# Performance work log

Measured on AMD Instinct MI355X. Metric: run time of the kernel, lower is better.

Reference implementation:

```python
import jax, jax.numpy as jnp
import numpy as np

# Faithful JAX translation of fastmax_function with mask=True, p=1, normalize=0.
# In that branch the torch code sets temperature = 1 and uses a0 = a1 = 1.

def setup_inputs() -> dict:
    key = jax.random.key(0)
    kq, kk, kv = jax.random.split(key, 3)
    b, h, n, d = 2, 8, 8192, 32
    q = jax.random.normal(kq, (b, h, n, d), dtype=jnp.float32)
    k = jax.random.normal(kk, (b, h, n, d), dtype=jnp.float32)
    v = jax.random.normal(kv, (b, h, n, d), dtype=jnp.float32)
    return {"q": q, "k": k, "v": v}


def reference(q, k, v):
    # q, k, v: (b, h, n, d); causal (mask=True), p=1, a0=a1=1, temperature=1
    b, h, n, d = q.shape
    # first term: running sum of values
    first = jnp.cumsum(v, axis=2)                                  # (b,h,n,d)
    # second term: q_i . (sum_{j<=i} k_j v_j^T)
    kv = jnp.einsum('bhnd,bhne->bhnde', k, v)                      # (b,h,n,d,d)
    kv_cs = jnp.cumsum(kv, axis=2)                                 # (b,h,n,d,d)
    second = jnp.einsum('bhnd,bhnde->bhne', q, kv_cs)              # (b,h,n,d)
    # denominator: i + q_i . (sum_{j<=i} k_j)
    k_cs = jnp.cumsum(k, axis=2)                                   # (b,h,n,d)
    div1 = jnp.arange(1, n + 1, dtype=q.dtype)                     # (n,)
    div2 = jnp.einsum('bhnd,bhnd->bhn', q, k_cs)                   # (b,h,n)
    div = (div1[None, None, :] + div2)[..., None]                  # (b,h,n,1)
    return (first + second) / div
```

## Files before the change

### kernel.cpp

```cpp
#include <hip/hip_runtime.h>


#define D      32
#define C      64
#define NCHUNK 128
#define BH     16
#define NSEQ   8192
#define STATE  1088

typedef __attribute__((ext_vector_type(8))) short bf16x8;
typedef __attribute__((ext_vector_type(4))) float f32x4;

__device__ __forceinline__ unsigned short f2bf(float x) {
  union { float f; unsigned u; } c; c.f = x;
  unsigned r = (c.u + 0x7FFFu + ((c.u >> 16) & 1u)) >> 16;
  return (unsigned short)r;
}

__global__ __launch_bounds__(256) void chunk_state_kernel(
    const float* __restrict__ k, const float* __restrict__ v,
    float* __restrict__ states) {
  int blk = blockIdx.x;
  int bh  = blk >> 7;
  int c   = blk & 127;
  size_t off = ((size_t)bh * NSEQ + (size_t)c * C) * D;
  const float* kp = k + off;
  const float* vp = v + off;

  __shared__ __align__(16) unsigned short kT[D * 72];
  __shared__ __align__(16) unsigned short vT[D * 72];
  __shared__ __align__(16) float psK[256];
  __shared__ __align__(16) float psV[256];

  int t = threadIdx.x;
  int e = t & 31;
  float sk = 0.f, sv = 0.f;
  for (int r = 0; r < 8; ++r) {
    int idx = t + r * 256;
    int j = idx >> 5;
    float kvv = kp[idx], vvv = vp[idx];
    kT[e * 72 + j] = f2bf(kvv);
    vT[e * 72 + j] = f2bf(vvv);
    sk += kvv; sv += vvv;
  }
  psK[t] = sk; psV[t] = sv;
  __syncthreads();

  int lane = t & 63, w = t >> 6;
  int m16 = lane & 15, quad = lane >> 4;
  int mb = w >> 1, nb = w & 1;
  f32x4 acc = {0.f, 0.f, 0.f, 0.f};
#pragma unroll
  for (int kb = 0; kb < 2; ++kb) {
    bf16x8 a = *(const bf16x8*)&kT[(16 * mb + m16) * 72 + kb * 32 + quad * 8];
    bf16x8 b = *(const bf16x8*)&vT[(16 * nb + m16) * 72 + kb * 32 + quad * 8];
    acc = __builtin_amdgcn_mfma_f32_16x16x32_bf16(a, b, acc, 0, 0, 0);
  }
  float* st = states + (size_t)blk * STATE;
#pragma unroll
  for (int reg = 0; reg < 4; ++reg) {
    int d1 = 16 * mb + quad * 4 + reg;
    int d2 = 16 * nb + m16;
    st[d1 * 32 + d2] = acc[reg];
  }
  if (t < 64) {
    int ee = t & 31;
    float s = 0.f;
    if (t < 32) {
#pragma unroll
      for (int g = 0; g < 8; ++g) s += psK[ee + 32 * g];
      st[1024 + ee] = s;
    } else {
#pragma unroll
      for (int g = 0; g < 8; ++g) s += psV[ee + 32 * g];
      st[1056 + ee] = s;
    }
  }
}

__global__ __launch_bounds__(256) void scan_kernel(float* __restrict__ states) {
  int gidx = blockIdx.x * 256 + threadIdx.x;
  int bh = gidx / STATE;
  int e  = gidx % STATE;
  float* base = states + (size_t)bh * NCHUNK * STATE + e;
  float a = 0.f;
#pragma unroll 1
  for (int c0 = 0; c0 < NCHUNK; c0 += 16) {
    float s[16];
#pragma unroll
    for (int r = 0; r < 16; ++r) s[r] = base[(size_t)(c0 + r) * STATE];
#pragma unroll
    for (int r = 0; r < 16; ++r) { float tv = s[r]; s[r] = a; a += tv; }
#pragma unroll
    for (int r = 0; r < 16; ++r) base[(size_t)(c0 + r) * STATE] = s[r];
  }
}

__global__ __launch_bounds__(256) void output_kernel(
    const float* __restrict__ q, const float* __restrict__ k,
    const float* __restrict__ v, const float* __restrict__ states,
    float* __restrict__ out) {
  int blk = blockIdx.x;
  int bh  = blk >> 7;
  int c   = blk & 127;
  size_t off = ((size_t)bh * NSEQ + (size_t)c * C) * D;
  const float* qp = q + off;
  const float* kp = k + off;
  const float* vp = v + off;
  const float* st = states + (size_t)blk * STATE;

  __shared__ __align__(16) unsigned short qbf[C * 40];
  __shared__ __align__(16) unsigned short kbf[C * 40];
  __shared__ __align__(16) unsigned short vTbf[D * 72];
  __shared__ __align__(16) unsigned short kvTbf[D * 40];
  __shared__ __align__(16) unsigned short Tbf[C * 72];
  __shared__ __align__(16) float q_s[C * 36];
  __shared__ __align__(16) float kc_s[C * 36];
  __shared__ __align__(16) float gtot[8 * 32];
  __shared__ __align__(16) float kpre_s[D], vpre_s[D], invdiv_s[C];

  int t = threadIdx.x;
  int e = t & 31;

  for (int z = t; z < (C * 72) / 8; z += 256)
    ((uint4*)Tbf)[z] = make_uint4(0, 0, 0, 0);
  for (int r = 0; r < 8; ++r) {
    int idx = t + r * 256;
    int j = idx >> 5;
    float qv = qp[idx], kv = kp[idx], vv = vp[idx];
    q_s[j * 36 + e]  = qv;  qbf[j * 40 + e] = f2bf(qv);
    kc_s[j * 36 + e] = kv;  kbf[j * 40 + e] = f2bf(kv);
    vTbf[e * 72 + j] = f2bf(vv);
  }
  for (int r = 0; r < 4; ++r) {
    int idx = t + r * 256;
    int dd = idx >> 5;
    kvTbf[e * 40 + dd] = f2bf(st[idx]);
  }
  if (t < 32)      kpre_s[t]      = st[1024 + t];
  else if (t < 64) vpre_s[t - 32] = st[1024 + t];
  __syncthreads();

  int lane = t & 63, w = t >> 6;
  int m16 = lane & 15, quad = lane >> 4;

  const bf16x8 aQ = *(const bf16x8*)&qbf[(16 * w + m16) * 40 + quad * 8];
  for (int jb = 0; jb <= w; ++jb) {
    bf16x8 bK = *(const bf16x8*)&kbf[(16 * jb + m16) * 40 + quad * 8];
    f32x4 cS = {0.f, 0.f, 0.f, 0.f};
    cS = __builtin_amdgcn_mfma_f32_16x16x32_bf16(aQ, bK, cS, 0, 0, 0);
    int jcol = 16 * jb + m16;
#pragma unroll
    for (int reg = 0; reg < 4; ++reg) {
      int i = 16 * w + quad * 4 + reg;
      float tv = (jcol <= i) ? (1.f + cS[reg]) : 0.f;
      Tbf[i * 72 + jcol] = f2bf(tv);
    }
  }
  int rg = t >> 5;
  float vals[8];
  {
    float run = 0.f;
#pragma unroll
    for (int r = 0; r < 8; ++r) {
      vals[r] = kc_s[(rg * 8 + r) * 36 + e];
      run += vals[r];
    }
    gtot[rg * 32 + e] = run;
  }
  __syncthreads();

  {
    float offv = kpre_s[e];
    for (int g = 0; g < rg; ++g) offv += gtot[g * 32 + e];
    float cacc = offv;
#pragma unroll
    for (int r = 0; r < 8; ++r) {
      cacc += vals[r];
      kc_s[(rg * 8 + r) * 36 + e] = cacc;
    }
  }
  __syncthreads();

  if (t < 64) {
    int i = t;
    float dp = 0.f;
#pragma unroll
    for (int d4 = 0; d4 < 8; ++d4) {
      float4 qv = *(const float4*)&q_s[i * 36 + 4 * d4];
      float4 kc = *(const float4*)&kc_s[i * 36 + 4 * d4];
      dp += qv.x * kc.x + qv.y * kc.y + qv.z * kc.z + qv.w * kc.w;
    }
    invdiv_s[i] = 1.f / ((float)(c * C + i + 1) + dp);
  }
  f32x4 o0 = {0.f, 0.f, 0.f, 0.f}, o1 = {0.f, 0.f, 0.f, 0.f};
  {
    bf16x8 b0 = *(const bf16x8*)&kvTbf[(m16)      * 40 + quad * 8];
    bf16x8 b1 = *(const bf16x8*)&kvTbf[(16 + m16) * 40 + quad * 8];
    o0 = __builtin_amdgcn_mfma_f32_16x16x32_bf16(aQ, b0, o0, 0, 0, 0);
    o1 = __builtin_amdgcn_mfma_f32_16x16x32_bf16(aQ, b1, o1, 0, 0, 0);
  }
  int kbcnt = (w >= 2) ? 2 : 1;
  for (int kb = 0; kb < kbcnt; ++kb) {
    bf16x8 aT = *(const bf16x8*)&Tbf[(16 * w + m16) * 72 + kb * 32 + quad * 8];
    bf16x8 b0 = *(const bf16x8*)&vTbf[(m16)      * 72 + kb * 32 + quad * 8];
    bf16x8 b1 = *(const bf16x8*)&vTbf[(16 + m16) * 72 + kb * 32 + quad * 8];
    o0 = __builtin_amdgcn_mfma_f32_16x16x32_bf16(aT, b0, o0, 0, 0, 0);
    o1 = __builtin_amdgcn_mfma_f32_16x16x32_bf16(aT, b1, o1, 0, 0, 0);
  }
  __syncthreads();

#pragma unroll
  for (int reg = 0; reg < 4; ++reg) {
    int i = 16 * w + quad * 4 + reg;
    float id = invdiv_s[i];
    int e0 = m16, e1 = 16 + m16;
    out[off + (size_t)i * D + e0] = (vpre_s[e0] + o0[reg]) * id;
    out[off + (size_t)i * D + e1] = (vpre_s[e1] + o1[reg]) * id;
  }
}

extern "C" void kernel_launch(void* const* d_in, const int* in_sizes, int n_in,
                              void* d_out, int out_size, void* d_ws, size_t ws_size,
                              hipStream_t stream) {
  const float* q = (const float*)d_in[0];
  const float* k = (const float*)d_in[1];
  const float* v = (const float*)d_in[2];
  float* out    = (float*)d_out;
  float* states = (float*)d_ws;

  chunk_state_kernel<<<BH * NCHUNK, 256, 0, stream>>>(k, v, states);
  scan_kernel<<<(BH * STATE) / 256, 256, 0, stream>>>(states);
  output_kernel<<<BH * NCHUNK, 256, 0, stream>>>(q, k, v, states, out);
}
```

Before: 113.3 us.

## Vectorize global loads with float4 and permute value columns for paired float2 stores

Both chunk kernels now load q/k/v and states as float4 vectors with a row/column-group thread mapping instead of scalar strided loads, and write bf16 tiles to shared memory in vector form. The value and kv-state columns are permuted so each lane's two MFMA output columns are adjacent, which allows float2 output stores. The scan kernel is unrolled to 32 chunks per batch, and the partial-sum reduction is reorganized to match the new mapping. The aim is fewer, wider memory transactions, at the cost of a slightly more complex indexing scheme.

```diff
diff --git a/kernel.cpp b/kernel.cpp
--- a/kernel.cpp
+++ b/kernel.cpp
@@ -10,6 +10,7 @@
 
 typedef __attribute__((ext_vector_type(8))) short bf16x8;
 typedef __attribute__((ext_vector_type(4))) float f32x4;
+typedef __attribute__((ext_vector_type(4))) unsigned short u16x4;
 
 __device__ __forceinline__ unsigned short f2bf(float x) {
   union { float f; unsigned u; } c; c.f = x;
@@ -17,33 +18,39 @@
   return (unsigned short)r;
 }
 
+__device__ __forceinline__ int permcol(int e) {
+  return (e & 1) ? (16 + (e >> 1)) : (e >> 1);
+}
+
 __global__ __launch_bounds__(256) void chunk_state_kernel(
     const float* __restrict__ k, const float* __restrict__ v,
     float* __restrict__ states) {
   int blk = blockIdx.x;
-  int bh  = blk >> 7;
-  int c   = blk & 127;
-  size_t off = ((size_t)bh * NSEQ + (size_t)c * C) * D;
-  const float* kp = k + off;
-  const float* vp = v + off;
+  const float4* kp = (const float4*)k + (size_t)blk * 512;
+  const float4* vp = (const float4*)v + (size_t)blk * 512;
 
   __shared__ __align__(16) unsigned short kT[D * 72];
   __shared__ __align__(16) unsigned short vT[D * 72];
-  __shared__ __align__(16) float psK[256];
-  __shared__ __align__(16) float psV[256];
-
-  int t = threadIdx.x;
-  int e = t & 31;
-  float sk = 0.f, sv = 0.f;
-  for (int r = 0; r < 8; ++r) {
-    int idx = t + r * 256;
-    int j = idx >> 5;
-    float kvv = kp[idx], vvv = vp[idx];
-    kT[e * 72 + j] = f2bf(kvv);
-    vT[e * 72 + j] = f2bf(vvv);
-    sk += kvv; sv += vvv;
-  }
-  psK[t] = sk; psV[t] = sv;
+  __shared__ __align__(16) float4 psK[256];
+  __shared__ __align__(16) float4 psV[256];
+
+  int t  = threadIdx.x;
+  int j0 = t >> 3;
+  int cb = (t & 7) * 4;
+  float4 kA = kp[t], kB = kp[t + 256];
+  float4 vA = vp[t], vB = vp[t + 256];
+
+  const float* ka = &kA.x; const float* kb = &kB.x;
+  const float* va = &vA.x; const float* vb = &vB.x;
+#pragma unroll
+  for (int cc = 0; cc < 4; ++cc) {
+    kT[(cb + cc) * 72 + j0]      = f2bf(ka[cc]);
+    kT[(cb + cc) * 72 + j0 + 32] = f2bf(kb[cc]);
+    vT[(cb + cc) * 72 + j0]      = f2bf(va[cc]);
+    vT[(cb + cc) * 72 + j0 + 32] = f2bf(vb[cc]);
+  }
+  psK[t] = make_float4(kA.x + kB.x, kA.y + kB.y, kA.z + kB.z, kA.w + kB.w);
+  psV[t] = make_float4(vA.x + vB.x, vA.y + vB.y, vA.z + vB.z, vA.w + vB.w);
   __syncthreads();
 
   int lane = t & 63, w = t >> 6;
@@ -51,9 +58,9 @@
   int mb = w >> 1, nb = w & 1;
   f32x4 acc = {0.f, 0.f, 0.f, 0.f};
 #pragma unroll
-  for (int kb = 0; kb < 2; ++kb) {
-    bf16x8 a = *(const bf16x8*)&kT[(16 * mb + m16) * 72 + kb * 32 + quad * 8];
-    bf16x8 b = *(const bf16x8*)&vT[(16 * nb + m16) * 72 + kb * 32 + quad * 8];
+  for (int kb2 = 0; kb2 < 2; ++kb2) {
+    bf16x8 a = *(const bf16x8*)&kT[(16 * mb + m16) * 72 + kb2 * 32 + quad * 8];
+    bf16x8 b = *(const bf16x8*)&vT[(16 * nb + m16) * 72 + kb2 * 32 + quad * 8];
     acc = __builtin_amdgcn_mfma_f32_16x16x32_bf16(a, b, acc, 0, 0, 0);
   }
   float* st = states + (size_t)blk * STATE;
@@ -65,16 +72,11 @@
   }
   if (t < 64) {
     int ee = t & 31;
+    const float* ps = (t < 32) ? (const float*)psK : (const float*)psV;
     float s = 0.f;
-    if (t < 32) {
-#pragma unroll
-      for (int g = 0; g < 8; ++g) s += psK[ee + 32 * g];
-      st[1024 + ee] = s;
-    } else {
-#pragma unroll
-      for (int g = 0; g < 8; ++g) s += psV[ee + 32 * g];
-      st[1056 + ee] = s;
-    }
+#pragma unroll
+    for (int m = 0; m < 32; ++m) s += ps[ee + 32 * m];
+    st[1024 + ((t < 32) ? ee : 32 + ee)] = s;
   }
 }
 
@@ -85,14 +87,14 @@
   float* base = states + (size_t)bh * NCHUNK * STATE + e;
   float a = 0.f;
 #pragma unroll 1
-  for (int c0 = 0; c0 < NCHUNK; c0 += 16) {
-    float s[16];
-#pragma unroll
-    for (int r = 0; r < 16; ++r) s[r] = base[(size_t)(c0 + r) * STATE];
-#pragma unroll
-    for (int r = 0; r < 16; ++r) { float tv = s[r]; s[r] = a; a += tv; }
-#pragma unroll
-    for (int r = 0; r < 16; ++r) base[(size_t)(c0 + r) * STATE] = s[r];
+  for (int c0 = 0; c0 < NCHUNK; c0 += 32) {
+    float s[32];
+#pragma unroll
+    for (int r = 0; r < 32; ++r) s[r] = base[(size_t)(c0 + r) * STATE];
+#pragma unroll
+    for (int r = 0; r < 32; ++r) { float tv = s[r]; s[r] = a; a += tv; }
+#pragma unroll
+    for (int r = 0; r < 32; ++r) base[(size_t)(c0 + r) * STATE] = s[r];
   }
 }
 
@@ -101,13 +103,12 @@
     const float* __restrict__ v, const float* __restrict__ states,
     float* __restrict__ out) {
   int blk = blockIdx.x;
-  int bh  = blk >> 7;
   int c   = blk & 127;
-  size_t off = ((size_t)bh * NSEQ + (size_t)c * C) * D;
-  const float* qp = q + off;
-  const float* kp = k + off;
-  const float* vp = v + off;
-  const float* st = states + (size_t)blk * STATE;
+  size_t off = (size_t)blk * (C * D);
+  const float4* qp4 = (const float4*)q + (size_t)blk * 512;
+  const float4* kp4 = (const float4*)k + (size_t)blk * 512;
+  const float4* vp4 = (const float4*)v + (size_t)blk * 512;
+  const float4* st4 = (const float4*)(states + (size_t)blk * STATE);
 
   __shared__ __align__(16) unsigned short qbf[C * 40];
   __shared__ __align__(16) unsigned short kbf[C * 40];
@@ -119,26 +120,45 @@
   __shared__ __align__(16) float gtot[8 * 32];
   __shared__ __align__(16) float kpre_s[D], vpre_s[D], invdiv_s[C];
 
-  int t = threadIdx.x;
-  int e = t & 31;
+  int t  = threadIdx.x;
+  int j0 = t >> 3;
+  int cb = (t & 7) * 4;
+
+  float4 qA = qp4[t], qB = qp4[t + 256];
+  float4 kA = kp4[t], kB = kp4[t + 256];
+  float4 vA = vp4[t], vB = vp4[t + 256];
+  float4 sv = st4[t];
+  float4 tail = make_float4(0.f, 0.f, 0.f, 0.f);
+  if (t < 16) tail = st4[256 + t];
 
   for (int z = t; z < (C * 72) / 8; z += 256)
     ((uint4*)Tbf)[z] = make_uint4(0, 0, 0, 0);
-  for (int r = 0; r < 8; ++r) {
-    int idx = t + r * 256;
-    int j = idx >> 5;
-    float qv = qp[idx], kv = kp[idx], vv = vp[idx];
-    q_s[j * 36 + e]  = qv;  qbf[j * 40 + e] = f2bf(qv);
-    kc_s[j * 36 + e] = kv;  kbf[j * 40 + e] = f2bf(kv);
-    vTbf[e * 72 + j] = f2bf(vv);
-  }
-  for (int r = 0; r < 4; ++r) {
-    int idx = t + r * 256;
-    int dd = idx >> 5;
-    kvTbf[e * 40 + dd] = f2bf(st[idx]);
-  }
-  if (t < 32)      kpre_s[t]      = st[1024 + t];
-  else if (t < 64) vpre_s[t - 32] = st[1024 + t];
+
+  *(float4*)&q_s[j0 * 36 + cb]        = qA;
+  *(float4*)&q_s[(j0 + 32) * 36 + cb] = qB;
+  *(float4*)&kc_s[j0 * 36 + cb]        = kA;
+  *(float4*)&kc_s[(j0 + 32) * 36 + cb] = kB;
+  *(u16x4*)&qbf[j0 * 40 + cb] =
+      (u16x4){f2bf(qA.x), f2bf(qA.y), f2bf(qA.z), f2bf(qA.w)};
+  *(u16x4*)&qbf[(j0 + 32) * 40 + cb] =
+      (u16x4){f2bf(qB.x), f2bf(qB.y), f2bf(qB.z), f2bf(qB.w)};
+  *(u16x4*)&kbf[j0 * 40 + cb] =
+      (u16x4){f2bf(kA.x), f2bf(kA.y), f2bf(kA.z), f2bf(kA.w)};
+  *(u16x4*)&kbf[(j0 + 32) * 40 + cb] =
+      (u16x4){f2bf(kB.x), f2bf(kB.y), f2bf(kB.z), f2bf(kB.w)};
+  {
+    const float* va = &vA.x; const float* vb = &vB.x;
+    const float* sp = &sv.x;
+#pragma unroll
+    for (int cc = 0; cc < 4; ++cc) {
+      int n = permcol(cb + cc);
+      vTbf[n * 72 + j0]      = f2bf(va[cc]);
+      vTbf[n * 72 + j0 + 32] = f2bf(vb[cc]);
+      kvTbf[n * 40 + j0]     = f2bf(sp[cc]);
+    }
+  }
+  if (t < 8)            ((float4*)kpre_s)[t]     = tail;
+  else if (t < 16)      ((float4*)vpre_s)[t - 8] = tail;
   __syncthreads();
 
   int lane = t & 63, w = t >> 6;
@@ -158,6 +178,7 @@
     }
   }
   int rg = t >> 5;
+  int e  = t & 31;
   float vals[8];
   {
     float run = 0.f;
@@ -210,13 +231,15 @@
   }
   __syncthreads();
 
+  int e0 = 2 * m16;
 #pragma unroll
   for (int reg = 0; reg < 4; ++reg) {
     int i = 16 * w + quad * 4 + reg;
     float id = invdiv_s[i];
-    int e0 = m16, e1 = 16 + m16;
-    out[off + (size_t)i * D + e0] = (vpre_s[e0] + o0[reg]) * id;
-    out[off + (size_t)i * D + e1] = (vpre_s[e1] + o1[reg]) * id;
+    float2 o;
+    o.x = (vpre_s[e0]     + o0[reg]) * id;
+    o.y = (vpre_s[e0 + 1] + o1[reg]) * id;
+    *(float2*)&out[off + (size_t)i * D + e0] = o;
   }
 }
 
```

Result: faster. 108.9 us (-3.9%).
